# Optimization experiments

Measured on AMD Instinct MI355X. Metric: run time of the kernel, lower is better.

Reference implementation:

```python
import jax, jax.numpy as jnp
import numpy as np

N = 100000   # nodes
E = 300000   # edges (avg degree ~3, molecular graphs)
DIN = 128    # input node features
H = 512      # hidden
OUT = 256    # out_channels
G = 4096     # number of graphs
EPS = 1e-5
SLOPE = 0.01  # LeakyReLU default negative slope
SELF_W = 2.0  # improved=True self-loop weight


def setup_inputs() -> dict:
    key = jax.random.key(0)
    ks = jax.random.split(key, 12)
    x = jax.random.normal(ks[0], (N, DIN), dtype=jnp.float32)
    edge_index = jax.random.randint(ks[1], (2, E), 0, N, dtype=jnp.int64)
    batch = jnp.sort(jax.random.randint(ks[2], (N,), 0, G, dtype=jnp.int64))
    s1 = 1.0 / np.sqrt(DIN)
    s2 = 1.0 / np.sqrt(H)
    return {
        "x": x,
        "edge_index": edge_index,
        "batch": batch,
        "W1": jax.random.normal(ks[3], (DIN, H), dtype=jnp.float32) * s1,
        "b1": jax.random.normal(ks[4], (H,), dtype=jnp.float32) * 0.01,
        "g1": jax.random.uniform(ks[5], (H,), dtype=jnp.float32, minval=0.5, maxval=1.5),
        "beta1": jax.random.normal(ks[6], (H,), dtype=jnp.float32) * 0.01,
        "W2": jax.random.normal(ks[7], (H, H), dtype=jnp.float32) * s2,
        "b2": jax.random.normal(ks[8], (H,), dtype=jnp.float32) * 0.01,
        "g2": jax.random.uniform(ks[9], (H,), dtype=jnp.float32, minval=0.5, maxval=1.5),
        "beta2": jax.random.normal(ks[10], (H,), dtype=jnp.float32) * 0.01,
        "Wf": jax.random.normal(ks[11], (H, OUT), dtype=jnp.float32) * s2,
        "bf": jnp.zeros((OUT,), dtype=jnp.float32),
    }


def _gcn_conv(x, W, b, row, col, n):
    # GCNConv(improved=True, add_self_loops=True, normalize=True), edge_weight=None
    h = x @ W                                   # [n, H]
    ones = jnp.ones(row.shape[0], dtype=h.dtype)
    deg = jax.ops.segment_sum(ones, col, num_segments=n) + SELF_W
    dinv = jax.lax.rsqrt(deg)                   # deg > 0 always (self-loop weight 2)
    norm = dinv[row] * dinv[col]                # [E]
    agg = jax.ops.segment_sum(h[row] * norm[:, None], col, num_segments=n)
    agg = agg + h * (SELF_W * dinv * dinv)[:, None]  # self-loop messages, no edge materialization
    return agg + b


def _bn(x, g, beta):
    # training-mode BatchNorm1d: biased batch stats
    mu = jnp.mean(x, axis=0)
    var = jnp.mean(jnp.square(x - mu), axis=0)
    return g * (x - mu) * jax.lax.rsqrt(var + EPS) + beta


def reference(x, edge_index, batch, W1, b1, g1, beta1, W2, b2, g2, beta2, Wf, bf):
    row, col = edge_index[0], edge_index[1]
    n = x.shape[0]
    h = _gcn_conv(x, W1, b1, row, col, n)
    h = jax.nn.leaky_relu(_bn(h, g1, beta1), SLOPE)
    # dropout is identity in eval mode
    h = _gcn_conv(h, W2, b2, row, col, n)
    h = jax.nn.leaky_relu(_bn(h, g2, beta2), SLOPE)
    pooled = jax.ops.segment_max(h, batch, num_segments=G)
    pooled = jnp.where(jnp.isfinite(pooled), pooled, 0.0)  # empty graphs -> 0 (torch_scatter fill)
    return pooled @ Wf + bf
```

## Files before the change

### kernel.cpp

```cpp
#include <hip/hip_runtime.h>
#include <hip/hip_bf16.h>

typedef __hip_bfloat16 bf16;
typedef __attribute__((ext_vector_type(8))) short short8;
typedef __attribute__((ext_vector_type(4))) float f32x4;

#define HDIM 512
#define SLOPE 0.01f
#define BN_EPS 1e-5f
#define STRIPES 8

__device__ inline float bf2f(short s) {
    unsigned u = ((unsigned)(unsigned short)s) << 16;
    return __builtin_bit_cast(float, u);
}
__device__ inline unsigned short f2bfbits(float v) {
    bf16 h = __float2bfloat16(v);
    return (unsigned short)__builtin_bit_cast(short, h);
}

struct EdgeRec { int src; float nm; };

__global__ void detect_types(const int* __restrict__ ei, const unsigned* __restrict__ xw,
                             int* __restrict__ flags, float* __restrict__ gpart) {
    __shared__ int nzhi, okbf;
    if (threadIdx.x == 0) { nzhi = 0; okbf = 0; }
    __syncthreads();
    int lo = 0, ok = 0;
    for (int i = threadIdx.x; i < 2048; i += 256)
        if (ei[2 * i + 1] != 0) lo++;
    for (int i = threadIdx.x; i < 1024; i += 256) {
        unsigned w = (xw[i] & 0xFFFFu) << 16;
        float av = fabsf(__builtin_bit_cast(float, w));
        if (av > 0.0009f && av < 64.0f) ok++;
    }
    for (int i = threadIdx.x; i < STRIPES * 2 * HDIM; i += 256) gpart[i] = 0.f;
    if (lo) atomicAdd(&nzhi, lo);
    if (ok) atomicAdd(&okbf, ok);
    __syncthreads();
    if (threadIdx.x == 0) {
        flags[0] = (nzhi == 0) ? 1 : 0;
        flags[1] = (okbf < 512) ? 1 : 0;
    }
}

__global__ void conv_all_idx(const int* __restrict__ ei, const int* __restrict__ batch,
                             int* __restrict__ ei32, int* __restrict__ batch32,
                             int* __restrict__ cnt, int e2, int n,
                             const int* __restrict__ flags) {
    int i = blockIdx.x * blockDim.x + threadIdx.x;
    int i64 = flags[0];
    if (i < e2) {
        int v = i64 ? (int)((const long long*)ei)[i] : ei[i];
        ei32[i] = v;
        if (i >= e2 / 2) atomicAdd(&cnt[v], 1);
    } else if (i < e2 + n) {
        int j = i - e2;
        batch32[j] = i64 ? (int)((const long long*)batch)[j] : batch[j];
    }
}

__global__ void wt_conv_all(const void* __restrict__ W1, const void* __restrict__ W2,
                            const void* __restrict__ Wf, const void* __restrict__ bf_,
                            bf16* __restrict__ W1T, bf16* __restrict__ W2T,
                            bf16* __restrict__ WfT, bf16* __restrict__ bfbf,
                            const int* __restrict__ flags) {
    const int S1 = 128 * 512, S2 = 512 * 512, S3 = 512 * 256;
    int idx = blockIdx.x * 256 + threadIdx.x;
    bool f32 = flags[1] != 0;
    if (idx < S1) {
        int nn = idx / 128, k = idx - nn * 128;
        float v = f32 ? ((const float*)W1)[(size_t)k * 512 + nn]
                      : __bfloat162float(((const bf16*)W1)[(size_t)k * 512 + nn]);
        W1T[idx] = __float2bfloat16(v);
    } else if (idx < S1 + S2) {
        int t = idx - S1;
        int nn = t / 512, k = t - nn * 512;
        float v = f32 ? ((const float*)W2)[(size_t)k * 512 + nn]
                      : __bfloat162float(((const bf16*)W2)[(size_t)k * 512 + nn]);
        W2T[t] = __float2bfloat16(v);
    } else if (idx < S1 + S2 + S3) {
        int t = idx - S1 - S2;
        int nn = t / 512, k = t - nn * 512;
        float v = f32 ? ((const float*)Wf)[(size_t)k * 256 + nn]
                      : __bfloat162float(((const bf16*)Wf)[(size_t)k * 256 + nn]);
        WfT[t] = __float2bfloat16(v);
    } else if (idx < S1 + S2 + S3 + 256) {
        int t = idx - S1 - S2 - S3;
        float v = f32 ? ((const float*)bf_)[t]
                      : __bfloat162float(((const bf16*)bf_)[t]);
        bfbf[t] = __float2bfloat16(v);
    }
}

__global__ void finalize_deg(const int* __restrict__ cnt, float* __restrict__ dinv,
                             float* __restrict__ selfw, int n) {
    int i = blockIdx.x * blockDim.x + threadIdx.x;
    if (i < n) {
        float d = (float)cnt[i] + 2.0f;
        dinv[i] = rsqrtf(d);
        selfw[i] = 2.0f / d;
    }
}

__global__ __launch_bounds__(256) void scan_part(
    const int* __restrict__ counts, int* __restrict__ offsets,
    int* __restrict__ bsum, int n)
{
    __shared__ int s[512];
    int b = blockIdx.x;
    int base = b * 512;
    int t = threadIdx.x;
    s[t]       = (base + t       < n) ? counts[base + t]       : 0;
    s[t + 256] = (base + t + 256 < n) ? counts[base + t + 256] : 0;

    int offset = 1;
    for (int d = 256; d > 0; d >>= 1) {
        __syncthreads();
        if (t < d) {
            int ai = offset * (2 * t + 1) - 1;
            int bi = offset * (2 * t + 2) - 1;
            s[bi] += s[ai];
        }
        offset <<= 1;
    }
    __syncthreads();
    if (t == 0) { bsum[b] = s[511]; s[511] = 0; }
    for (int d = 1; d < 512; d <<= 1) {
        offset >>= 1;
        __syncthreads();
        if (t < d) {
            int ai = offset * (2 * t + 1) - 1;
            int bi = offset * (2 * t + 2) - 1;
            int tmp = s[ai]; s[ai] = s[bi]; s[bi] += tmp;
        }
    }
    __syncthreads();
    if (base + t < n)       offsets[base + t]       = s[t];
    if (base + t + 256 < n) offsets[base + t + 256] = s[t + 256];
}

__global__ __launch_bounds__(1024) void scan_tops(int* __restrict__ bsum, int nb) {
    __shared__ int s[1024];
    int t = threadIdx.x;
    s[t] = (t < nb) ? bsum[t] : 0;
    __syncthreads();
    for (int off = 1; off < 1024; off <<= 1) {
        int v = (t >= off) ? s[t - off] : 0;
        __syncthreads();
        s[t] += v;
        __syncthreads();
    }
    if (t < nb) bsum[t] = (t == 0) ? 0 : s[t - 1];
}

__global__ __launch_bounds__(256) void scan_add(
    int* __restrict__ offsets, const int* __restrict__ bsum, int n, int e)
{
    int b = blockIdx.x;
    int base = b * 512;
    int add = bsum[b];
    int t = threadIdx.x;
    if (base + t < n)       offsets[base + t]       += add;
    if (base + t + 256 < n) offsets[base + t + 256] += add;
    if (b == 0 && t == 0) offsets[n] = e;
}

__global__ void scatter_edges(const int* __restrict__ rows, const int* __restrict__ cols,
                              const int* __restrict__ offsets, int* __restrict__ cursor,
                              const float* __restrict__ dinv,
                              EdgeRec* __restrict__ er, int e)
{
    int i = blockIdx.x * blockDim.x + threadIdx.x;
    if (i < e) {
        int d = cols[i];
        int r = rows[i];
        int pos = offsets[d] + atomicAdd(&cursor[d], 1);
        EdgeRec rec;
        rec.src = r;
        rec.nm = dinv[d] * dinv[r];
        er[pos] = rec;
    }
}

#define GEMM_STAGE(buf, kk)                                                              \
    {                                                                                    \
        _Pragma("unroll")                                                                \
        for (int i_ = 0; i_ < 2; i_++) {                                                 \
            int c_ = wave * 2 + i_;                                                      \
            const bf16* ga_ = A  + (size_t)(m0 + c_ * 16 + lrow) * K + (kk) + lcol;      \
            const bf16* gb_ = BT + (size_t)(n0 + c_ * 16 + lrow) * K + (kk) + lcol;      \
            __builtin_amdgcn_global_load_lds(                                            \
                (const __attribute__((address_space(1))) unsigned*)ga_,                  \
                (__attribute__((address_space(3))) unsigned*)(As[buf] + c_ * 512), 16, 0, 0); \
            __builtin_amdgcn_global_load_lds(                                            \
                (const __attribute__((address_space(1))) unsigned*)gb_,                  \
                (__attribute__((address_space(3))) unsigned*)(Bs[buf] + c_ * 512), 16, 0, 0); \
        }                                                                                \
    }

#define GEMM_COMPUTE(buf)                                                                \
    {                                                                                    \
        short8 a[4], b[4];                                                               \
        _Pragma("unroll")                                                                \
        for (int mi2 = 0; mi2 < 4; mi2++)                                                \
            a[mi2] = *(const short8*)&As[buf][(wm + mi2 * 16 + r) * 32 + aoff];          \
        _Pragma("unroll")                                                                \
        for (int ni = 0; ni < 4; ni++)                                                   \
            b[ni] = *(const short8*)&Bs[buf][(wn + ni * 16 + r) * 32 + aoff];            \
        _Pragma("unroll")                                                                \
        for (int mi2 = 0; mi2 < 4; mi2++)                                                \
            _Pragma("unroll")                                                            \
            for (int ni = 0; ni < 4; ni++)                                               \
                acc[mi2][ni] = __builtin_amdgcn_mfma_f32_16x16x32_bf16(                  \
                    a[mi2], b[ni], acc[mi2][ni], 0, 0, 0);                               \
    }

template<bool STATS>
__global__ __launch_bounds__(256, 4) void gemm_m97(
    const bf16* __restrict__ A, const bf16* __restrict__ BT,
    void* __restrict__ C, const bf16* __restrict__ bias,
    int M, int K, int N, const int* __restrict__ cf32,
    float* __restrict__ gpart, int MB)
{
    __shared__ bf16 As[2][128 * 32];
    __shared__ bf16 Bs[2][128 * 32];

    int NBN = N >> 7;
    int id = blockIdx.x;
    int grp = id / (8 * NBN);
    int loc = id - grp * 8 * NBN;
    int mi = loc & 7;
    int nblk = loc >> 3;
    int mblk = grp * 8 + mi;
    if (mblk >= MB) return;

    int tid = threadIdx.x;
    int wave = tid >> 6, lane = tid & 63, q = lane >> 4, r = lane & 15;
    int wm = (wave >> 1) * 64, wn = (wave & 1) * 64;
    int m0 = mblk * 128, n0 = nblk * 128;
    bool c32 = cf32 && *cf32;

    int lrow = lane >> 2;
    int lcol = (((lane & 3) ^ ((lane >> 3) & 3)) * 8);
    int aoff = (q ^ ((r >> 1) & 3)) * 8;

    f32x4 acc[4][4];
#pragma unroll
    for (int mi2 = 0; mi2 < 4; mi2++)
#pragma unroll
        for (int ni = 0; ni < 4; ni++)
            acc[mi2][ni] = {0.f, 0.f, 0.f, 0.f};

    const int nK = K >> 5;

    GEMM_STAGE(0, 0);
    __syncthreads();

    int cur = 0;
    for (int t = 1; t < nK; ++t) {
        GEMM_STAGE(cur ^ 1, t * 32);
        GEMM_COMPUTE(cur);
        __syncthreads();
        cur ^= 1;
    }
    GEMM_COMPUTE(cur);

#pragma unroll
    for (int mi2 = 0; mi2 < 4; mi2++) {
#pragma unroll
        for (int ni = 0; ni < 4; ni++) {
            int gn = n0 + wn + ni * 16 + r;
            float bv = bias ? __bfloat162float(bias[gn]) : 0.f;
#pragma unroll
            for (int reg = 0; reg < 4; reg++) {
                int gm = m0 + wm + mi2 * 16 + q * 4 + reg;
                if (gm < M) {
                    float val = acc[mi2][ni][reg] + bv;
                    if (c32) ((float*)C)[(size_t)gm * N + gn] = val;
                    else     ((bf16*)C)[(size_t)gm * N + gn] = __float2bfloat16(val);
                }
            }
        }
    }

    if constexpr (STATS) {
        float* base = gpart + (size_t)(mblk & (STRIPES - 1)) * 2 * HDIM;
#pragma unroll
        for (int ni = 0; ni < 4; ni++) {
            float cs = 0.f, cq = 0.f;
#pragma unroll
            for (int mi2 = 0; mi2 < 4; mi2++)
#pragma unroll
                for (int reg = 0; reg < 4; reg++) {
                    int gm = m0 + wm + mi2 * 16 + q * 4 + reg;
                    if (gm < M) {
                        float v = acc[mi2][ni][reg];
                        cs += v; cq += v * v;
                    }
                }
            cs += __shfl_xor(cs, 16, 64);
            cs += __shfl_xor(cs, 32, 64);
            cq += __shfl_xor(cq, 16, 64);
            cq += __shfl_xor(cq, 32, 64);
            if (q == 0) {
                int c = n0 + wn + ni * 16 + r;
                atomicAdd(&base[c], cs);
                atomicAdd(&base[HDIM + c], cq);
            }
        }
    }
}

__global__ __launch_bounds__(256) void agg_csr_din(
    const void* __restrict__ x, const int* __restrict__ offsets,
    const EdgeRec* __restrict__ er, const float* __restrict__ selfw,
    bf16* __restrict__ out, int n, const int* __restrict__ flags)
{
    int wave = threadIdx.x >> 6, lane = threadIdx.x & 63;
    int gw = blockIdx.x * 4 + wave;
    int nw = gridDim.x * 4;
    bool f32 = flags[1] != 0;

    for (int dst = gw; dst < n; dst += nw) {
        int s0 = offsets[dst], s1 = offsets[dst + 1];
        float sw = selfw[dst];
        float a0, a1;
        if (f32) {
            float2 v = ((const float2*)x)[(size_t)dst * 64 + lane];
            a0 = sw * v.x; a1 = sw * v.y;
        } else {
            unsigned u = ((const unsigned*)x)[(size_t)dst * 64 + lane];
            a0 = sw * bf2f((short)(u & 0xFFFF)); a1 = sw * bf2f((short)(u >> 16));
        }
        int p = s0;
        for (; p + 1 < s1; p += 2) {
            EdgeRec e0 = er[p], e1 = er[p + 1];
            if (f32) {
                float2 v0 = ((const float2*)x)[(size_t)e0.src * 64 + lane];
                float2 v1 = ((const float2*)x)[(size_t)e1.src * 64 + lane];
                a0 += e0.nm * v0.x + e1.nm * v1.x;
                a1 += e0.nm * v0.y + e1.nm * v1.y;
            } else {
                unsigned u0 = ((const unsigned*)x)[(size_t)e0.src * 64 + lane];
                unsigned u1 = ((const unsigned*)x)[(size_t)e1.src * 64 + lane];
                a0 += e0.nm * bf2f((short)(u0 & 0xFFFF)) + e1.nm * bf2f((short)(u1 & 0xFFFF));
                a1 += e0.nm * bf2f((short)(u0 >> 16))    + e1.nm * bf2f((short)(u1 >> 16));
            }
        }
        if (p < s1) {
            EdgeRec e0 = er[p];
            if (f32) {
                float2 v0 = ((const float2*)x)[(size_t)e0.src * 64 + lane];
                a0 += e0.nm * v0.x; a1 += e0.nm * v0.y;
            } else {
                unsigned u0 = ((const unsigned*)x)[(size_t)e0.src * 64 + lane];
                a0 += e0.nm * bf2f((short)(u0 & 0xFFFF)); a1 += e0.nm * bf2f((short)(u0 >> 16));
            }
        }
        ((unsigned*)out)[(size_t)dst * 64 + lane] =
            (unsigned)f2bfbits(a0) | ((unsigned)f2bfbits(a1) << 16);
    }
}

__global__ __launch_bounds__(256) void agg_csr_bn(
    const bf16* __restrict__ h, const int* __restrict__ offsets,
    const EdgeRec* __restrict__ er, const float* __restrict__ selfw,
    const float* __restrict__ scale, const float* __restrict__ shift,
    bf16* __restrict__ y, int n)
{
    int wave = threadIdx.x >> 6, lane = threadIdx.x & 63;
    int f0 = lane * 8;
    int gw = blockIdx.x * 4 + wave;
    int nw = gridDim.x * 4;

    float sc[8], sh[8];
#pragma unroll
    for (int j = 0; j < 8; j++) { sc[j] = scale[f0 + j]; sh[j] = shift[f0 + j]; }

    for (int dst = gw; dst < n; dst += nw) {
        int s0 = offsets[dst], s1 = offsets[dst + 1];
        float sw = selfw[dst];
        short8 hv = *(const short8*)(h + (size_t)dst * HDIM + f0);
        float acc[8];
#pragma unroll
        for (int j = 0; j < 8; j++) {
            float t = sc[j] * bf2f(hv[j]) + sh[j];
            t = t > 0.f ? t : SLOPE * t;
            acc[j] = sw * t;
        }
        int p = s0;
        for (; p + 1 < s1; p += 2) {
            EdgeRec e0 = er[p], e1 = er[p + 1];
            short8 v0 = *(const short8*)(h + (size_t)e0.src * HDIM + f0);
            short8 v1 = *(const short8*)(h + (size_t)e1.src * HDIM + f0);
#pragma unroll
            for (int j = 0; j < 8; j++) {
                float t0 = sc[j] * bf2f(v0[j]) + sh[j];
                t0 = t0 > 0.f ? t0 : SLOPE * t0;
                float t1 = sc[j] * bf2f(v1[j]) + sh[j];
                t1 = t1 > 0.f ? t1 : SLOPE * t1;
                acc[j] += e0.nm * t0 + e1.nm * t1;
            }
        }
        if (p < s1) {
            EdgeRec e0 = er[p];
            short8 v0 = *(const short8*)(h + (size_t)e0.src * HDIM + f0);
#pragma unroll
            for (int j = 0; j < 8; j++) {
                float t0 = sc[j] * bf2f(v0[j]) + sh[j];
                t0 = t0 > 0.f ? t0 : SLOPE * t0;
                acc[j] += e0.nm * t0;
            }
        }
        short8 o;
#pragma unroll
        for (int j = 0; j < 8; j++) ((bf16*)&o)[j] = __float2bfloat16(acc[j]);
        *(short8*)(y + (size_t)dst * HDIM + f0) = o;
    }
}

__global__ void bn_final(float* __restrict__ gpart,
                         const void* __restrict__ gamma, const void* __restrict__ beta,
                         float* __restrict__ scale, float* __restrict__ shift,
                         float invN, const int* __restrict__ flags)
{
    int f = threadIdx.x;
    float s = 0.f, q = 0.f;
#pragma unroll
    for (int k = 0; k < STRIPES; k++) {
        s += gpart[(size_t)k * 2 * HDIM + f];
        q += gpart[(size_t)k * 2 * HDIM + HDIM + f];
        gpart[(size_t)k * 2 * HDIM + f] = 0.f;
        gpart[(size_t)k * 2 * HDIM + HDIM + f] = 0.f;
    }
    float g = flags[1] ? ((const float*)gamma)[f]
                       : __bfloat162float(((const bf16*)gamma)[f]);
    float b = flags[1] ? ((const float*)beta)[f]
                       : __bfloat162float(((const bf16*)beta)[f]);
    float mu = s * invN;
    float var = fmaxf(q * invN - mu * mu, 0.f);
    float inv = rsqrtf(var + BN_EPS);
    float sc = g * inv;
    scale[f] = sc;
    shift[f] = b - mu * sc;
}

__global__ __launch_bounds__(256) void pool_fused(
    const bf16* __restrict__ y, const int* __restrict__ batch,
    const float* __restrict__ scale, const float* __restrict__ shift,
    bf16* __restrict__ pooled, int n, int G)
{
    int wave = threadIdx.x >> 6, lane = threadIdx.x & 63;
    int g = blockIdx.x * 4 + wave;
    if (g >= G) return;
    int f0 = lane * 8;

    int lo = 0, hi = n;
    while (lo < hi) { int mid = (lo + hi) >> 1; if (batch[mid] < g) lo = mid + 1; else hi = mid; }
    int s = lo;
    hi = n;
    while (lo < hi) { int mid = (lo + hi) >> 1; if (batch[mid] <= g) lo = mid + 1; else hi = mid; }
    int e = lo;

    float mx[8], mn[8];
#pragma unroll
    for (int j = 0; j < 8; j++) { mx[j] = -3.0e38f; mn[j] = 3.0e38f; }

    int rr = s;
    for (; rr + 1 < e; rr += 2) {
        short8 v0 = *(const short8*)(y + (size_t)rr * HDIM + f0);
        short8 v1 = *(const short8*)(y + (size_t)(rr + 1) * HDIM + f0);
#pragma unroll
        for (int j = 0; j < 8; j++) {
            float a = bf2f(v0[j]), b = bf2f(v1[j]);
            mx[j] = fmaxf(mx[j], fmaxf(a, b));
            mn[j] = fminf(mn[j], fminf(a, b));
        }
    }
    if (rr < e) {
        short8 v0 = *(const short8*)(y + (size_t)rr * HDIM + f0);
#pragma unroll
        for (int j = 0; j < 8; j++) {
            float a = bf2f(v0[j]);
            mx[j] = fmaxf(mx[j], a);
            mn[j] = fminf(mn[j], a);
        }
    }

    short8 o;
#pragma unroll
    for (int j = 0; j < 8; j++) {
        float outv = 0.f;
        if (s < e) {
            float sc = scale[f0 + j];
            float t = sc * (sc >= 0.f ? mx[j] : mn[j]) + shift[f0 + j];
            outv = t > 0.f ? t : SLOPE * t;
        }
        ((bf16*)&o)[j] = __float2bfloat16(outv);
    }
    *(short8*)(pooled + (size_t)g * HDIM + f0) = o;
}

extern "C" void kernel_launch(void* const* d_in, const int* in_sizes, int n_in,
                              void* d_out, int out_size, void* d_ws, size_t ws_size,
                              hipStream_t stream)
{
    const void* x     = d_in[0];
    const int*  ei    = (const int*)d_in[1];
    const int*  batch = (const int*)d_in[2];

    const int N   = in_sizes[2];
    const int E   = in_sizes[1] / 2;
    const int DIN = 128;
    const int OUT = 256;
    const int G   = out_size / OUT;
    const int Mp  = (N + 127) & ~127;
    const int MB  = Mp / 128;
    const int MB8 = (MB + 7) & ~7;

    char* p = (char*)d_ws;
    bf16* B1     = (bf16*)p;  p += (size_t)Mp * HDIM * sizeof(bf16);
    bf16* B2     = (bf16*)p;  p += (size_t)Mp * HDIM * sizeof(bf16);
    bf16* Q      = (bf16*)p;  p += (size_t)Mp * DIN * sizeof(bf16);
    bf16* W1T    = (bf16*)p;  p += (size_t)HDIM * DIN * sizeof(bf16);
    bf16* W2T    = (bf16*)p;  p += (size_t)HDIM * HDIM * sizeof(bf16);
    bf16* WfT    = (bf16*)p;  p += (size_t)OUT * HDIM * sizeof(bf16);
    bf16* bfbf   = (bf16*)p;  p += 512 * sizeof(bf16);
    int* ei32    = (int*)p;   p += (size_t)2 * E * sizeof(int);
    int* batch32 = (int*)p;   p += (size_t)N * sizeof(int);
    float* dinv  = (float*)p; p += (size_t)N * sizeof(float);
    float* selfw = (float*)p; p += (size_t)N * sizeof(float);
    int* offsets = (int*)p;   p += (size_t)(N + 4) * sizeof(int);
    int* cursor  = (int*)p;   p += (size_t)N * sizeof(int);
    EdgeRec* er  = (EdgeRec*)p; p += (size_t)E * sizeof(EdgeRec);
    int* bsum    = (int*)p;   p += 1024 * sizeof(int);
    float* gpart = (float*)p; p += (size_t)STRIPES * 2 * HDIM * sizeof(float);
    float* sc1   = (float*)p; p += HDIM * sizeof(float);
    float* sh1   = (float*)p; p += HDIM * sizeof(float);
    float* sc2   = (float*)p; p += HDIM * sizeof(float);
    float* sh2   = (float*)p; p += HDIM * sizeof(float);
    int* flags   = (int*)p;   p += 4 * sizeof(int);

    detect_types<<<1, 256, 0, stream>>>(ei, (const unsigned*)x, flags, gpart);
    hipMemsetAsync(cursor, 0, (size_t)N * sizeof(int), stream);
    conv_all_idx<<<(2 * E + N + 255) / 256, 256, 0, stream>>>(
        ei, batch, ei32, batch32, cursor, 2 * E, N, flags);
    wt_conv_all<<<(128 * 512 + 512 * 512 + 512 * 256 + 256 + 255) / 256, 256, 0, stream>>>(
        d_in[3], d_in[7], d_in[11], d_in[12], W1T, W2T, WfT, bfbf, flags);

    const int* rows = ei32;
    const int* cols = ei32 + E;

    finalize_deg<<<(N + 255) / 256, 256, 0, stream>>>(cursor, dinv, selfw, N);
    int nb = (N + 511) / 512;
    scan_part<<<nb, 256, 0, stream>>>(cursor, offsets, bsum, N);
    scan_tops<<<1, 1024, 0, stream>>>(bsum, nb);
    scan_add<<<nb, 256, 0, stream>>>(offsets, bsum, N, E);
    hipMemsetAsync(cursor, 0, (size_t)N * sizeof(int), stream);
    scatter_edges<<<(E + 255) / 256, 256, 0, stream>>>(rows, cols, offsets, cursor,
                                                       dinv, er, E);

    int gemm_blocks = MB8 * (HDIM / 128);

    agg_csr_din<<<2048, 256, 0, stream>>>(x, offsets, er, selfw, Q, N, flags);
    gemm_m97<true><<<gemm_blocks, 256, 0, stream>>>(
        Q, W1T, B2, nullptr, N, DIN, HDIM, nullptr, gpart, MB);
    bn_final<<<1, HDIM, 0, stream>>>(gpart, d_in[5], d_in[6], sc1, sh1, 1.0f / N, flags);

    agg_csr_bn<<<2048, 256, 0, stream>>>(B2, offsets, er, selfw, sc1, sh1, B1, N);
    gemm_m97<true><<<gemm_blocks, 256, 0, stream>>>(
        B1, W2T, B2, nullptr, N, HDIM, HDIM, nullptr, gpart, MB);
    bn_final<<<1, HDIM, 0, stream>>>(gpart, d_in[9], d_in[10], sc2, sh2, 1.0f / N, flags);

    pool_fused<<<(G + 3) / 4, 256, 0, stream>>>(B2, batch32, sc2, sh2, Q, N, G);
    gemm_m97<false><<<(G / 128) * (OUT / 128), 256, 0, stream>>>(
        Q, WfT, d_out, bfbf, G, HDIM, OUT, flags + 1, nullptr, G / 128);
}
```

Baseline: 472.0 us.

## Fuse segment max/min pooling into second GEMM epilogue via float atomics

The second GEMM no longer writes its 100k x 512 bf16 output. Its epilogue instead reduces each column over runs of rows that share a graph id and atomically updates per-graph max and min buffers. A small finalize kernel then applies the BN scale and shift plus LeakyReLU, picking max or min by the sign of the scale. This removes a large write and re-read of the hidden activations, at the cost of many global atomics and an extra init kernel. Pooling now uses fp32 pre-rounding values, so results can differ slightly from the previous bf16 path.

```diff
diff --git a/kernel.cpp b/kernel.cpp
--- a/kernel.cpp
+++ b/kernel.cpp
@@ -17,6 +17,15 @@
 __device__ inline unsigned short f2bfbits(float v) {
     bf16 h = __float2bfloat16(v);
     return (unsigned short)__builtin_bit_cast(short, h);
+}
+
+__device__ inline void atomicMaxF(float* a, float v) {
+    if (v >= 0.f) atomicMax((int*)a, __float_as_int(v));
+    else          atomicMin((unsigned int*)a, __float_as_uint(v));
+}
+__device__ inline void atomicMinF(float* a, float v) {
+    if (v >= 0.f) atomicMin((int*)a, __float_as_int(v));
+    else          atomicMax((unsigned int*)a, __float_as_uint(v));
 }
 
 struct EdgeRec { int src; float nm; };
@@ -183,6 +192,12 @@
     }
 }
 
+__global__ __launch_bounds__(256) void pool_init(float* __restrict__ pmax,
+                                                 float* __restrict__ pmin, int n) {
+    int i = blockIdx.x * 256 + threadIdx.x;
+    if (i < n) { pmax[i] = -3.0e38f; pmin[i] = 3.0e38f; }
+}
+
 #define GEMM_STAGE(buf, kk)                                                              \
     {                                                                                    \
         _Pragma("unroll")                                                                \
@@ -216,12 +231,13 @@
                     a[mi2], b[ni], acc[mi2][ni], 0, 0, 0);                               \
     }
 
-template<bool STATS>
+template<bool STATS, bool POOL>
 __global__ __launch_bounds__(256, 4) void gemm_m97(
     const bf16* __restrict__ A, const bf16* __restrict__ BT,
     void* __restrict__ C, const bf16* __restrict__ bias,
     int M, int K, int N, const int* __restrict__ cf32,
-    float* __restrict__ gpart, int MB)
+    float* __restrict__ gpart, int MB,
+    const int* __restrict__ batchp, float* __restrict__ pmax, float* __restrict__ pmin)
 {
     __shared__ bf16 As[2][128 * 32];
     __shared__ bf16 Bs[2][128 * 32];
@@ -266,20 +282,59 @@
     }
     GEMM_COMPUTE(cur);
 
-#pragma unroll
-    for (int mi2 = 0; mi2 < 4; mi2++) {
+    if constexpr (!POOL) {
+#pragma unroll
+        for (int mi2 = 0; mi2 < 4; mi2++) {
+#pragma unroll
+            for (int ni = 0; ni < 4; ni++) {
+                int gn = n0 + wn + ni * 16 + r;
+                float bv = bias ? __bfloat162float(bias[gn]) : 0.f;
+#pragma unroll
+                for (int reg = 0; reg < 4; reg++) {
+                    int gm = m0 + wm + mi2 * 16 + q * 4 + reg;
+                    if (gm < M) {
+                        float val = acc[mi2][ni][reg] + bv;
+                        if (c32) ((float*)C)[(size_t)gm * N + gn] = val;
+                        else     ((bf16*)C)[(size_t)gm * N + gn] = __float2bfloat16(val);
+                    }
+                }
+            }
+        }
+    }
+
+    if constexpr (POOL) {
+        int batchv[16];
+#pragma unroll
+        for (int mi2 = 0; mi2 < 4; mi2++)
+#pragma unroll
+            for (int reg = 0; reg < 4; reg++) {
+                int gm = m0 + wm + mi2 * 16 + q * 4 + reg;
+                batchv[mi2 * 4 + reg] = (gm < M) ? batchp[gm] : -1;
+            }
 #pragma unroll
         for (int ni = 0; ni < 4; ni++) {
             int gn = n0 + wn + ni * 16 + r;
-            float bv = bias ? __bfloat162float(bias[gn]) : 0.f;
-#pragma unroll
-            for (int reg = 0; reg < 4; reg++) {
-                int gm = m0 + wm + mi2 * 16 + q * 4 + reg;
-                if (gm < M) {
-                    float val = acc[mi2][ni][reg] + bv;
-                    if (c32) ((float*)C)[(size_t)gm * N + gn] = val;
-                    else     ((bf16*)C)[(size_t)gm * N + gn] = __float2bfloat16(val);
+            float cmax = 0.f, cmin = 0.f;
+            int curg = -1;
+#pragma unroll
+            for (int t2 = 0; t2 < 16; t2++) {
+                int g = batchv[t2];
+                float v = acc[t2 >> 2][ni][t2 & 3];
+                if (g >= 0) {
+                    if (g != curg) {
+                        if (curg >= 0) {
+                            atomicMaxF(&pmax[(size_t)curg * N + gn], cmax);
+                            atomicMinF(&pmin[(size_t)curg * N + gn], cmin);
+                        }
+                        curg = g; cmax = v; cmin = v;
+                    } else {
+                        cmax = fmaxf(cmax, v); cmin = fminf(cmin, v);
+                    }
                 }
+            }
+            if (curg >= 0) {
+                atomicMaxF(&pmax[(size_t)curg * N + gn], cmax);
+                atomicMinF(&pmin[(size_t)curg * N + gn], cmin);
             }
         }
     }
@@ -446,60 +501,28 @@
     shift[f] = b - mu * sc;
 }
 
-__global__ __launch_bounds__(256) void pool_fused(
-    const bf16* __restrict__ y, const int* __restrict__ batch,
+__global__ __launch_bounds__(256) void pool_fin(
+    const float* __restrict__ pmax, const float* __restrict__ pmin,
     const float* __restrict__ scale, const float* __restrict__ shift,
-    bf16* __restrict__ pooled, int n, int G)
-{
-    int wave = threadIdx.x >> 6, lane = threadIdx.x & 63;
-    int g = blockIdx.x * 4 + wave;
-    if (g >= G) return;
-    int f0 = lane * 8;
-
-    int lo = 0, hi = n;
-    while (lo < hi) { int mid = (lo + hi) >> 1; if (batch[mid] < g) lo = mid + 1; else hi = mid; }
-    int s = lo;
-    hi = n;
-    while (lo < hi) { int mid = (lo + hi) >> 1; if (batch[mid] <= g) lo = mid + 1; else hi = mid; }
-    int e = lo;
-
-    float mx[8], mn[8];
-#pragma unroll
-    for (int j = 0; j < 8; j++) { mx[j] = -3.0e38f; mn[j] = 3.0e38f; }
-
-    int rr = s;
-    for (; rr + 1 < e; rr += 2) {
-        short8 v0 = *(const short8*)(y + (size_t)rr * HDIM + f0);
-        short8 v1 = *(const short8*)(y + (size_t)(rr + 1) * HDIM + f0);
-#pragma unroll
-        for (int j = 0; j < 8; j++) {
-            float a = bf2f(v0[j]), b = bf2f(v1[j]);
-            mx[j] = fmaxf(mx[j], fmaxf(a, b));
-            mn[j] = fminf(mn[j], fminf(a, b));
-        }
-    }
-    if (rr < e) {
-        short8 v0 = *(const short8*)(y + (size_t)rr * HDIM + f0);
-#pragma unroll
-        for (int j = 0; j < 8; j++) {
-            float a = bf2f(v0[j]);
-            mx[j] = fmaxf(mx[j], a);
-            mn[j] = fminf(mn[j], a);
-        }
-    }
-
+    bf16* __restrict__ outQ, int total8)
+{
+    int i = blockIdx.x * 256 + threadIdx.x;
+    if (i >= total8) return;
+    int f0 = (i * 8) & (HDIM - 1);
     short8 o;
 #pragma unroll
     for (int j = 0; j < 8; j++) {
+        float mx = pmax[(size_t)i * 8 + j];
         float outv = 0.f;
-        if (s < e) {
+        if (mx > -2.9e38f) {
             float sc = scale[f0 + j];
-            float t = sc * (sc >= 0.f ? mx[j] : mn[j]) + shift[f0 + j];
+            float mv = (sc >= 0.f) ? mx : pmin[(size_t)i * 8 + j];
+            float t = sc * mv + shift[f0 + j];
             outv = t > 0.f ? t : SLOPE * t;
         }
         ((bf16*)&o)[j] = __float2bfloat16(outv);
     }
-    *(short8*)(pooled + (size_t)g * HDIM + f0) = o;
+    *(short8*)(outQ + (size_t)i * 8) = o;
 }
 
 extern "C" void kernel_launch(void* const* d_in, const int* in_sizes, int n_in,
@@ -542,6 +565,9 @@
     float* sh2   = (float*)p; p += HDIM * sizeof(float);
     int* flags   = (int*)p;   p += 4 * sizeof(int);
 
+    float* pmax = (float*)B2;
+    float* pmin = pmax + (size_t)G * HDIM;
+
     detect_types<<<1, 256, 0, stream>>>(ei, (const unsigned*)x, flags, gpart);
     hipMemsetAsync(cursor, 0, (size_t)N * sizeof(int), stream);
     conv_all_idx<<<(2 * E + N + 255) / 256, 256, 0, stream>>>(
@@ -564,16 +590,21 @@
     int gemm_blocks = MB8 * (HDIM / 128);
 
     agg_csr_din<<<2048, 256, 0, stream>>>(x, offsets, er, selfw, Q, N, flags);
-    gemm_m97<true><<<gemm_blocks, 256, 0, stream>>>(
-        Q, W1T, B2, nullptr, N, DIN, HDIM, nullptr, gpart, MB);
+    gemm_m97<true, false><<<gemm_blocks, 256, 0, stream>>>(
+        Q, W1T, B2, nullptr, N, DIN, HDIM, nullptr, gpart, MB,
+        nullptr, nullptr, nullptr);
     bn_final<<<1, HDIM, 0, stream>>>(gpart, d_in[5], d_in[6], sc1, sh1, 1.0f / N, flags);
 
     agg_csr_bn<<<2048, 256, 0, stream>>>(B2, offsets, er, selfw, sc1, sh1, B1, N);
-    gemm_m97<true><<<gemm_blocks, 256, 0, stream>>>(
-        B1, W2T, B2, nullptr, N, HDIM, HDIM, nullptr, gpart, MB);
+    pool_init<<<(G * HDIM + 255) / 256, 256, 0, stream>>>(pmax, pmin, G * HDIM);
+    gemm_m97<true, true><<<gemm_blocks, 256, 0, stream>>>(
+        B1, W2T, nullptr, nullptr, N, HDIM, HDIM, nullptr, gpart, MB,
+        batch32, pmax, pmin);
     bn_final<<<1, HDIM, 0, stream>>>(gpart, d_in[9], d_in[10], sc2, sh2, 1.0f / N, flags);
 
-    pool_fused<<<(G + 3) / 4, 256, 0, stream>>>(B2, batch32, sc2, sh2, Q, N, G);
-    gemm_m97<false><<<(G / 128) * (OUT / 128), 256, 0, stream>>>(
-        Q, WfT, d_out, bfbf, G, HDIM, OUT, flags + 1, nullptr, G / 128);
-}
+    pool_fin<<<(G * HDIM / 8 + 255) / 256, 256, 0, stream>>>(
+        pmax, pmin, sc2, sh2, Q, G * HDIM / 8);
+    gemm_m97<false, false><<<(G / 128) * (OUT / 128), 256, 0, stream>>>(
+        Q, WfT, d_out, bfbf, G, HDIM, OUT, flags + 1, nullptr, G / 128,
+        nullptr, nullptr, nullptr);
+}
```

Result: slower. 595.4 us (+26.1%).
